# Optimization experiments

Hardware: AMD Instinct MI355X
Metric: run time of the kernel (lower is better)

Reference implementation:

```python
import math
import jax, jax.numpy as jnp
import numpy as np
from jax import lax

N_HEADS = 8
FACTOR = 5


def _pos_emb(L, d):
    pos = jnp.arange(L, dtype=jnp.float32)[:, None]
    div = jnp.exp(jnp.arange(0, d, 2, dtype=jnp.float32) * (-math.log(10000.0) / d))
    pe = jnp.zeros((L, d), jnp.float32)
    pe = pe.at[:, 0::2].set(jnp.sin(pos * div))
    pe = pe.at[:, 1::2].set(jnp.cos(pos * div))
    return pe


def _circ_conv1d(x, w, b=None):
    # x: (B, L, Cin); w: torch conv1d weight (Cout, Cin, 3); circular padding=1
    xp = jnp.concatenate([x[:, -1:], x, x[:, :1]], axis=1)
    y = lax.conv_general_dilated(xp, jnp.transpose(w, (2, 1, 0)), (1,), 'VALID',
                                 dimension_numbers=('NWC', 'WIO', 'NWC'))
    return y + b if b is not None else y


def _ln(x, g, b, eps=1e-5):
    mu = x.mean(-1, keepdims=True)
    var = ((x - mu) ** 2).mean(-1, keepdims=True)
    return (x - mu) * lax.rsqrt(var + eps) * g + b


def _prob_attn(q, k, v, key):
    # q,k,v: (b, h, L, d); self-attention so l_q == l_k == L
    b, h, L, d = q.shape
    u = min(L, int(FACTOR * math.log(L + 1)))  # sample_k == n_top
    idx = jnp.asarray(jax.random.randint(key, (L, u), 0, L))  # shared across b,h as in torch

    # sampled QK scores: scan over the u samples to avoid a (b,h,L,u,d) gather blow-up
    def step(_, idx_s):
        kg = k[:, :, idx_s]  # (b,h,L,d): key idx_s[l] for query l
        return None, jnp.einsum('bhld,bhld->bhl', q, kg)
    _, qk = lax.scan(step, None, idx.T)  # (u, b, h, L)
    qk = jnp.moveaxis(qk, 0, -1)  # (b, h, L, u)

    m = qk.max(axis=-1) - qk.mean(axis=-1)  # sparsity measure, (b,h,L)
    _, top = lax.top_k(m, u)  # (b,h,u) top-u query indices

    q_red = jnp.take_along_axis(q, top[..., None], axis=2)  # (b,h,u,d)
    scores = jnp.einsum('bhud,bhkd->bhuk', q_red, k) * (1.0 / math.sqrt(d))
    attn = jax.nn.softmax(scores, axis=-1)
    ctx_top = jnp.einsum('bhuk,bhkd->bhud', attn, v)

    # non-selected queries get mean(V); scatter sparse-attention rows back in
    ctx = jnp.broadcast_to(v.mean(axis=2, keepdims=True), (b, h, L, d))
    bi = jnp.arange(b)[:, None, None]
    hi = jnp.arange(h)[None, :, None]
    return ctx.at[bi, hi, top].set(ctx_top)


def _attn_layer(x, wq, bq, wk, bk, wv, bv, wo, bo, key):
    b, L, dm = x.shape
    dh = dm // N_HEADS
    def split(w_, b_):
        return (x @ w_.T + b_).reshape(b, L, N_HEADS, dh).transpose(0, 2, 1, 3)
    ctx = _prob_attn(split(wq, bq), split(wk, bk), split(wv, bv), key)
    ctx = ctx.transpose(0, 2, 1, 3).reshape(b, L, dm)
    return ctx @ wo.T + bo


def _conv_layer(x, w, b, g, beta):
    # circular conv -> BatchNorm (batch stats, train-mode math) -> ELU -> maxpool k3 s2 p1
    y = _circ_conv1d(x, w, b)
    mu = y.mean(axis=(0, 1))
    var = y.var(axis=(0, 1))
    y = (y - mu) * lax.rsqrt(var + 1e-5) * g + beta
    y = jax.nn.elu(y)
    yp = jnp.pad(y, ((0, 0), (1, 1), (0, 0)), constant_values=-np.inf)
    return lax.reduce_window(yp, -np.inf, lax.max, (1, 3, 1), (1, 2, 1), 'VALID')


def _forward(x, skip_w, skip_b, token_conv_w, wq, bq, wk, bk, wv, bv, wo, bo,
             w1, b1, w2, b2, ln1_g, ln1_b, ln2_g, ln2_b,
             dc_w, dc_b, bn_g, bn_b, final_ln_g, final_ln_b, proj_w, proj_b):
    skip = x[:, -1] @ skip_w.T + skip_b  # (B, pred_len)
    h = _circ_conv1d(x, token_conv_w)  # token embedding (no bias)
    h = h + _pos_emb(h.shape[1], h.shape[2])
    E = wq.shape[0]
    base = jax.random.key(42)
    for i in range(E):
        new_h = _attn_layer(h, wq[i], bq[i], wk[i], bk[i], wv[i], bv[i], wo[i], bo[i],
                            jax.random.fold_in(base, i))
        h = h + new_h
        y = _ln(h, ln1_g[i], ln1_b[i])
        y = jax.nn.gelu(y @ w1[i].T + b1[i], approximate=False)  # conv1 is 1x1
        y = y @ w2[i].T + b2[i]  # conv2 is 1x1
        h = _ln(h + y, ln2_g[i], ln2_b[i])
        if i < E - 1:
            h = _conv_layer(h, dc_w[i], dc_b[i], bn_g[i], bn_b[i])  # halves L
    h = _ln(h, final_ln_g, final_ln_b)
    return h[:, -1] @ proj_w.T + proj_b + skip


def setup_inputs() -> dict:
    B, L, C_IN, D, DFF, E, P = 32, 2048, 7, 512, 2048, 3, 96
    key = jax.random.key(0)
    ks = iter(jax.random.split(key, 20))
    w = lambda shape: jax.random.normal(next(ks), shape, jnp.float32) * 0.02
    z = lambda shape: jnp.zeros(shape, jnp.float32)
    o = lambda shape: jnp.ones(shape, jnp.float32)
    return {
        'x': jax.random.normal(next(ks), (B, L, C_IN), jnp.float32),
        'skip_w': w((P, C_IN)), 'skip_b': z((P,)),
        'token_conv_w': w((D, C_IN, 3)),
        'wq': w((E, D, D)), 'bq': z((E, D)),
        'wk': w((E, D, D)), 'bk': z((E, D)),
        'wv': w((E, D, D)), 'bv': z((E, D)),
        'wo': w((E, D, D)), 'bo': z((E, D)),
        'w1': w((E, DFF, D)), 'b1': z((E, DFF)),
        'w2': w((E, D, DFF)), 'b2': z((E, D)),
        'ln1_g': o((E, D)), 'ln1_b': z((E, D)),
        'ln2_g': o((E, D)), 'ln2_b': z((E, D)),
        'dc_w': w((E - 1, D, D, 3)), 'dc_b': z((E - 1, D)),
        'bn_g': o((E - 1, D)), 'bn_b': z((E - 1, D)),
        'final_ln_g': o((D,)), 'final_ln_b': z((D,)),
        'proj_w': w((P, D)), 'proj_b': z((P,)),
    }


def reference(x, skip_w, skip_b, token_conv_w, wq, bq, wk, bk, wv, bv, wo, bo,
              w1, b1, w2, b2, ln1_g, ln1_b, ln2_g, ln2_b,
              dc_w, dc_b, bn_g, bn_b, final_ln_g, final_ln_b, proj_w, proj_b):
    return _forward(x, skip_w, skip_b, token_conv_w, wq, bq, wk, bk, wv, bv, wo, bo,
                    w1, b1, w2, b2, ln1_g, ln1_b, ln2_g, ln2_b,
                    dc_w, dc_b, bn_g, bn_b, final_ln_g, final_ln_b, proj_w, proj_b)
```

## Files before the change

kernel.cpp:

```cpp
#include <hip/hip_runtime.h>
#include <cmath>

#define DM 512
#define DH 64

typedef __attribute__((ext_vector_type(8))) short short8;
typedef __attribute__((ext_vector_type(4))) float float4v;

__device__ inline float b2f(unsigned short u){
  union{unsigned int i; float f;} z; z.i = ((unsigned)u)<<16; return z.f;
}
__device__ inline unsigned short f2b(float f){
  unsigned int x = __float_as_uint(f);
  return (unsigned short)((x + 0x7fffu + ((x>>16)&1u)) >> 16);
}
__device__ inline unsigned cvtpk2(float a, float b){
  unsigned r; asm("v_cvt_pk_bf16_f32 %0, %1, %2" : "=v"(r) : "v"(a), "v"(b)); return r;
}

#define GLL(gp, lp) __builtin_amdgcn_global_load_lds((const __attribute__((address_space(1))) void*)(gp), \
    (__attribute__((address_space(3))) void*)(lp), 16, 0, 0)

__host__ __device__ inline void tf2x32(unsigned k0, unsigned k1, unsigned& x0, unsigned& x1){
  const unsigned ks0=k0, ks1=k1, ks2=k0^k1^0x1BD11BDAu;
  x0 += ks0; x1 += ks1;
#define TF_ROT(r) { x0 += x1; x1 = (x1<<(r))|(x1>>(32-(r))); x1 ^= x0; }
  TF_ROT(13) TF_ROT(15) TF_ROT(26) TF_ROT(6)
  x0 += ks1; x1 += ks2 + 1u;
  TF_ROT(17) TF_ROT(29) TF_ROT(16) TF_ROT(24)
  x0 += ks2; x1 += ks0 + 2u;
  TF_ROT(13) TF_ROT(15) TF_ROT(26) TF_ROT(6)
  x0 += ks0; x1 += ks1 + 3u;
  TF_ROT(17) TF_ROT(29) TF_ROT(16) TF_ROT(24)
  x0 += ks1; x1 += ks2 + 4u;
  TF_ROT(13) TF_ROT(15) TF_ROT(26) TF_ROT(6)
  x0 += ks2; x1 += ks0 + 5u;
#undef TF_ROT
}

__global__ __launch_bounds__(256) void idx_kernel(int* __restrict__ idx, unsigned k2a, unsigned k2b,
                                                  int S2, int Lmask){
  int j = blockIdx.x*256 + threadIdx.x;
  if (j >= S2) return;
  unsigned x0 = (unsigned)j, x1 = (unsigned)(S2 + j);
  tf2x32(k2a, k2b, x0, x1);
  idx[j]      = (int)(x0 & (unsigned)Lmask);
  idx[S2 + j] = (int)(x1 & (unsigned)Lmask);
}

__global__ __launch_bounds__(256) void pe_kernel(float* __restrict__ pe, int L){
  int i = blockIdx.x*256 + threadIdx.x;
  int d = i % DM, l = i / DM;
  const float scale = -0.017988946f;
  float freq = expf((float)(d & ~1) * scale);
  float ang  = (float)l * freq;
  pe[i] = (d & 1) ? cosf(ang) : sinf(ang);
}

__global__ __launch_bounds__(256) void packtcw(const float* __restrict__ tcw, float* __restrict__ tcwT){
  int i = blockIdx.x*256 + threadIdx.x;
  if (i >= 21*DM) return;
  int j = i / DM, d = i % DM;
  tcwT[(size_t)j*DM + d] = tcw[(size_t)d*21 + (j%7)*3 + (j/7)];
}

__global__ __launch_bounds__(256) void embed2(const float* __restrict__ x, const float* __restrict__ tcwT,
                                              const float* __restrict__ pe, float* __restrict__ h, int L){
  int row = blockIdx.x; int l = row % L, b = row / L;
  __shared__ float xs[21];
  int t = threadIdx.x;
  if (t < 21){
    int c = t % 7, kk = t / 7;
    int ls = l + kk - 1; ls = (ls < 0) ? ls + L : (ls >= L ? ls - L : ls);
    xs[t] = x[((size_t)b*L + ls)*7 + c];
  }
  __syncthreads();
  for (int d = t; d < DM; d += 256){
    float acc = 0.f;
#pragma unroll
    for (int j=0;j<21;j++) acc += xs[j]*tcwT[j*DM + d];
    h[(size_t)row*DM + d] = acc + pe[(size_t)l*DM + d];
  }
}

__global__ __launch_bounds__(256) void f2b_vec(const float* __restrict__ src, unsigned short* __restrict__ dst, int n4){
  int i = blockIdx.x*256 + threadIdx.x;
  if (i >= n4) return;
  float4 v = ((const float4*)src)[i];
  uint2 o; o.x = cvtpk2(v.x, v.y); o.y = cvtpk2(v.z, v.w);
  ((uint2*)dst)[i] = o;
}

__global__ __launch_bounds__(256) void packconv(const float* __restrict__ dcw, unsigned short* __restrict__ wtapK){
  int i = blockIdx.x*256 + threadIdx.x;
  if (i >= 3*DM*DM) return;
  int n = i / (3*DM); int rem = i % (3*DM); int tap = rem / DM; int c = rem % DM;
  wtapK[(size_t)n*(3*DM) + tap*DM + c] = f2b(dcw[((size_t)n*DM + c)*3 + tap]);
}

__global__ __launch_bounds__(256) void catb_kernel(const float* __restrict__ a, const float* __restrict__ b,
    const float* __restrict__ c, float* __restrict__ o){
  int i = blockIdx.x*256 + threadIdx.x;
  if (i >= 1536) return;
  o[i] = (i < 512) ? a[i] : (i < 1024 ? b[i-512] : c[i-1024]);
}

template<int TN, int A32>
__global__ __launch_bounds__(256) void bgemm2(const void* __restrict__ Ain,
    const unsigned short* __restrict__ Wb, const float* __restrict__ bias, void* __restrict__ C,
    int N, int K, int L, int convmode, int act, int outbf, int qkv, size_t bufstride, int swz){
  constexpr int NJ = TN/32;
  constexpr int BR = TN/32;
  __shared__ unsigned short As[128*64];
  __shared__ unsigned short Bs[TN*64];
  int tid = threadIdx.x;
  int w = tid >> 6, ln = tid & 63;

  int bx = blockIdx.x, by = blockIdx.y;
  if (swz){
    int XT = gridDim.x, YT = gridDim.y;
    int lid = by*XT + bx;
    int xcd = lid & 7, s = lid >> 3;
    int ych = YT >> 3;
    int CHv = ych < swz ? ych : swz;
    int yloc = s % CHv;
    int t2 = s / CHv;
    int xx = t2 % XT;
    int chunk = t2 / XT;
    by = xcd*ych + chunk*CHv + yloc;
    bx = xx;
  }
  int row0 = by*128, col0 = bx*TN;
  int KA = convmode ? 512 : K;

  long aBase[4], dPrev[4], dNext[4]; int aCol[4];
#pragma unroll
  for (int g=0; g<4; g++){
    int ch = g*256 + tid;
    int r = ch >> 3, c = ch & 7;
    int gc = c ^ (r & 7);
    int gr = row0 + r;
    aCol[g] = gc*8;
    aBase[g] = (long)gr * KA;
    if (convmode){
      int l = gr % L;
      dPrev[g] = (l==0)   ? (long)(L-1)*KA : -(long)KA;
      dNext[g] = (l==L-1) ? -(long)(L-1)*KA : (long)KA;
    } else { dPrev[g]=0; dNext[g]=0; }
  }
  long bBase[BR];
#pragma unroll
  for (int g=0; g<BR; g++){
    int ch = g*256 + tid;
    int r = ch >> 3, c = ch & 7;
    int gc = c ^ (r & 7);
    bBase[g] = (long)(col0 + r)*K + gc*8;
  }
  int raBase[4], rbBase[NJ];
#pragma unroll
  for (int i=0;i<4;i++)  raBase[i] = ((w&1)*64 + i*16 + (ln&15))*8;
#pragma unroll
  for (int j=0;j<NJ;j++) rbBase[j] = ((w>>1)*(TN/2) + j*16 + (ln&15))*8;

  float4v acc[4][NJ] = {};
  int nIter = K/64;
  const unsigned short* A16 = (const unsigned short*)Ain;
  const float* Af = (const float*)Ain;

  for (int it=0; it<nIter; it++){
    int k0 = it*64;
    int kk = convmode ? (k0 & 511) : k0;
    int seg = convmode ? (k0 >> 9) : 1;
    if (A32){
#pragma unroll
      for (int g=0; g<4; g++){
        long d = convmode ? ((seg==0) ? dPrev[g] : (seg==2 ? dNext[g] : 0)) : 0;
        const float* src = Af + aBase[g] + d + kk + aCol[g];
        float4 v0 = *(const float4*)src;
        float4 v1 = *(const float4*)(src+4);
        uint4 pk;
        pk.x = cvtpk2(v0.x, v0.y); pk.y = cvtpk2(v0.z, v0.w);
        pk.z = cvtpk2(v1.x, v1.y); pk.w = cvtpk2(v1.z, v1.w);
        *(uint4*)((char*)As + g*4096 + tid*16) = pk;
      }
    } else {
#pragma unroll
      for (int g=0; g<4; g++){
        long d = convmode ? ((seg==0) ? dPrev[g] : (seg==2 ? dNext[g] : 0)) : 0;
        GLL(A16 + aBase[g] + d + kk + aCol[g], (char*)As + g*4096 + w*1024);
      }
    }
#pragma unroll
    for (int g=0; g<BR; g++)
      GLL(Wb + bBase[g] + k0, (char*)Bs + g*4096 + w*1024);
    __syncthreads();
    const char* ab = (const char*)As;
    const char* bb = (const char*)Bs;
#pragma unroll
    for (int s=0;s<2;s++){
      int xs = (s*4 + (ln>>4)) ^ (ln&7);
      short8 af[4], bf[NJ];
#pragma unroll
      for (int i=0;i<4;i++)  af[i] = *(const short8*)(ab + (raBase[i] + xs)*16);
#pragma unroll
      for (int j=0;j<NJ;j++) bf[j] = *(const short8*)(bb + (rbBase[j] + xs)*16);
#pragma unroll
      for (int i=0;i<4;i++)
#pragma unroll
        for (int j=0;j<NJ;j++)
          acc[i][j] = __builtin_amdgcn_mfma_f32_16x16x32_bf16(af[i], bf[j], acc[i][j], 0, 0, 0);
    }
    __syncthreads();
  }

  float* Cf = (float*)C;
  unsigned short* Cb = (unsigned short*)C;
  int colb0 = col0 + (w>>1)*(TN/2) + (ln & 15);
#pragma unroll
  for (int i=0;i<4;i++){
    int growb = row0 + (w&1)*64 + i*16 + (ln>>4)*4;
#pragma unroll
    for (int j=0;j<NJ;j++){
      int colb = colb0 + j*16;
      float vv[4];
#pragma unroll
      for (int r=0;r<4;r++){
        float v = acc[i][j][r];
        if (bias) v += bias[colb];
        if (act){
          float z = 0.7978845608f * v * (1.f + 0.044715f*v*v);
          float e = __expf(2.f*z);
          v = v * (1.f - 1.f/(e + 1.f));
        }
        vv[r] = v;
      }
      if (outbf){
        unsigned p01 = cvtpk2(vv[0], vv[1]);
        unsigned p23 = cvtpk2(vv[2], vv[3]);
        unsigned short h0 = (unsigned short)p01, h1 = (unsigned short)(p01>>16);
        unsigned short h2 = (unsigned short)p23, h3 = (unsigned short)(p23>>16);
        if (qkv){
          int bsel = colb >> 9;
          size_t base = (size_t)bsel*bufstride + (colb & 511);
          Cb[base + (size_t)(growb+0)*512] = h0;
          Cb[base + (size_t)(growb+1)*512] = h1;
          Cb[base + (size_t)(growb+2)*512] = h2;
          Cb[base + (size_t)(growb+3)*512] = h3;
        } else {
          Cb[(size_t)(growb+0)*N + colb] = h0;
          Cb[(size_t)(growb+1)*N + colb] = h1;
          Cb[(size_t)(growb+2)*N + colb] = h2;
          Cb[(size_t)(growb+3)*N + colb] = h3;
        }
      } else {
#pragma unroll
        for (int r=0;r<4;r++) Cf[(size_t)(growb+r)*N + colb] = vv[r];
      }
    }
  }
}

__global__ __launch_bounds__(256) void sample_m2(const unsigned short* __restrict__ q,
    const unsigned short* __restrict__ k, const int* __restrict__ idx, float* __restrict__ m, int L, int u){
  int w = (blockIdx.x*256 + threadIdx.x) >> 6;
  int lane = threadIdx.x & 63;
  int l = w % L; int b = w / L;
  const unsigned short* qrow = q + (size_t)w*DM + lane*8;
  uint4 qq = *(const uint4*)qrow;
  float qv[8];
  qv[0]=b2f((unsigned short)(qq.x&0xffff)); qv[1]=b2f((unsigned short)(qq.x>>16));
  qv[2]=b2f((unsigned short)(qq.y&0xffff)); qv[3]=b2f((unsigned short)(qq.y>>16));
  qv[4]=b2f((unsigned short)(qq.z&0xffff)); qv[5]=b2f((unsigned short)(qq.z>>16));
  qv[6]=b2f((unsigned short)(qq.w&0xffff)); qv[7]=b2f((unsigned short)(qq.w>>16));
  const unsigned short* kb = k + (size_t)b*L*DM + lane*8;
  const int* ip = idx + (size_t)l*u;
  float mx = -1e30f, sum = 0.f;
  for (int s=0; s<u; s++){
    int kp = ip[s];
    uint4 kk = *(const uint4*)(kb + (size_t)kp*DM);
    float p;
    p  = qv[0]*b2f((unsigned short)(kk.x&0xffff)) + qv[1]*b2f((unsigned short)(kk.x>>16));
    p += qv[2]*b2f((unsigned short)(kk.y&0xffff)) + qv[3]*b2f((unsigned short)(kk.y>>16));
    p += qv[4]*b2f((unsigned short)(kk.z&0xffff)) + qv[5]*b2f((unsigned short)(kk.z>>16));
    p += qv[6]*b2f((unsigned short)(kk.w&0xffff)) + qv[7]*b2f((unsigned short)(kk.w>>16));
    p += __shfl_xor(p, 1); p += __shfl_xor(p, 2); p += __shfl_xor(p, 4);
    mx = fmaxf(mx, p); sum += p;
  }
  if ((lane & 7) == 0){
    int hh = lane >> 3;
    m[((size_t)b*8 + hh)*L + l] = mx - sum/(float)u;
  }
}

template<int NS>
__global__ __launch_bounds__(256) void topk_kernel(const float* __restrict__ m, int* __restrict__ top, int L, int u){
  int bh = blockIdx.x;
  const float* mm = m + (size_t)bh*L;
  int t = threadIdx.x;
  float v[NS];
#pragma unroll
  for (int s=0; s<NS; s++) v[s] = mm[s*256 + t];
  __shared__ float rv[4];
  __shared__ int   ri[4];
  for (int it=0; it<u; it++){
    float bv = -1e30f; int bi = 0x7fffffff;
#pragma unroll
    for (int s=0; s<NS; s++){
      float x = v[s]; int i = s*256 + t;
      if (x > bv || (x == bv && i < bi)) { bv = x; bi = i; }
    }
#pragma unroll
    for (int off=32; off; off>>=1){
      float ov = __shfl_xor(bv, off); int oi = __shfl_xor(bi, off);
      if (ov > bv || (ov == bv && oi < bi)) { bv = ov; bi = oi; }
    }
    if ((t & 63) == 0){ rv[t>>6] = bv; ri[t>>6] = bi; }
    __syncthreads();
    bv = rv[0]; bi = ri[0];
#pragma unroll
    for (int k2=1; k2<4; k2++){
      float ov = rv[k2]; int oi = ri[k2];
      if (ov > bv || (ov == bv && oi < bi)) { bv = ov; bi = oi; }
    }
    if (t == 0) top[bh*u + it] = bi;
    if ((bi & 255) == t){
      int slot = bi >> 8;
#pragma unroll
      for (int s=0; s<NS; s++) if (s == slot) v[s] = -1e31f;
    }
    __syncthreads();
  }
}

#define CMC 32
__global__ __launch_bounds__(256) void colmean1(const float* __restrict__ src, float* __restrict__ part, int L){
  int b = blockIdx.x, ch = blockIdx.y;
  int rpb = L / CMC;
  int t = threadIdx.x;
  const float* p = src + ((size_t)b*L + (size_t)ch*rpb)*DM;
  float s0 = 0.f, s1 = 0.f;
  for (int r=0; r<rpb; r++){ s0 += p[(size_t)r*DM + t]; s1 += p[(size_t)r*DM + t + 256]; }
  float* o = part + ((size_t)b*CMC + ch)*DM;
  o[t] = s0; o[t+256] = s1;
}
__global__ __launch_bounds__(256) void colmean2(const float* __restrict__ part, float* __restrict__ dst, int L){
  int i = blockIdx.x*256 + threadIdx.x;
  int d = i % DM, b = i / DM;
  float s = 0.f;
  for (int c=0; c<CMC; c++) s += part[((size_t)b*CMC + c)*DM + d];
  dst[i] = s / (float)L;
}

__global__ __launch_bounds__(256) void tiny_gemm(const float* __restrict__ A, const float* __restrict__ W,
    const float* __restrict__ bias, float* __restrict__ C, int N, int K){
  int row = blockIdx.x;
  const float* ar = A + (size_t)row*K;
  __shared__ float as[DM];
  for (int k=threadIdx.x; k<K; k+=256) as[k] = ar[k];
  __syncthreads();
  for (int n = threadIdx.x; n < N; n += 256){
    float acc = bias ? bias[n] : 0.f;
    const float* wr = W + (size_t)n*K;
    for (int k=0; k<K; k++) acc += as[k]*wr[k];
    C[(size_t)row*N + n] = acc;
  }
}

__global__ __launch_bounds__(256) void qred_kernel(const unsigned short* __restrict__ q, const int* __restrict__ top,
    float* __restrict__ qred, int L, int u, int n){
  int i = blockIdx.x*256 + threadIdx.x;
  if (i >= n) return;
  int d = i & 63; int rest = i >> 6; int j = rest % u; int bh = rest / u;
  int hh = bh & 7; int b = bh >> 3;
  int pos = top[bh*u + j];
  qred[i] = b2f(q[((size_t)b*L + pos)*DM + hh*DH + d]);
}

#define FKT 128
__global__ __launch_bounds__(256) void flash_attn(const float* __restrict__ qred,
    const unsigned short* __restrict__ kbuf, const unsigned short* __restrict__ vbuf,
    float* __restrict__ partM, float* __restrict__ partL, float* __restrict__ partA,
    int L, int u, int KS){
  int ks = blockIdx.x, bh = blockIdx.y; int b = bh >> 3, h = bh & 7;
  int t = threadIdx.x;
  __shared__ float Qs[38*64];
  __shared__ unsigned short Ks[FKT*64];
  __shared__ unsigned short Vs[FKT*64];
  __shared__ float Ss[38*FKT];
  for (int i=t;i<u*64;i+=256) Qs[i] = qred[(size_t)bh*u*64 + i];
  int lane = t & 63, w = t >> 6;
  float rm[10], rl[10], racc[10];
#pragma unroll
  for (int j=0;j<10;j++){ rm[j]=-1e30f; rl[j]=0.f; racc[j]=0.f; }
  int nk = L / KS;
  int kbase = ks*nk;
  int key = t & 127, rh = t >> 7;
  for (int kt = 0; kt < nk; kt += FKT){
    __syncthreads();
    for (int e = t; e < FKT*8; e += 256){
      int k = e >> 3, c = e & 7;
      size_t gidx = ((size_t)(b*L + kbase + kt + k))*DM + h*DH + c*8;
      *(uint4*)((char*)Ks + (size_t)(k*8 + (c ^ (k&7)))*16) = *(const uint4*)(kbuf + gidx);
      *(uint4*)((char*)Vs + (size_t)e*16) = *(const uint4*)(vbuf + gidx);
    }
    __syncthreads();
    for (int r = rh; r < u; r += 2){
      const float4* q4 = (const float4*)(Qs + r*64);
      float acc = 0.f;
#pragma unroll
// ... 163 lines not shown
  int ch = blockIdx.x*256 + threadIdx.x;
  if (ch >= DM) return;
  float s = 0.f, q = 0.f;
  for (int mb=0; mb<NB; mb++){
    s += partS[(size_t)mb*DM + ch];
    q += partQ[(size_t)mb*DM + ch];
  }
  float mu = s / (float)M;
  stats[ch] = mu;
  stats[DM + ch] = q / (float)M - mu*mu;
}

__global__ __launch_bounds__(256) void bnpool(const unsigned short* __restrict__ C, const float* __restrict__ stats,
    const float* __restrict__ g, const float* __restrict__ bta, float* __restrict__ Out,
    int L, int Lo){
  size_t i = (size_t)blockIdx.x*256 + threadIdx.x;
  int ch = (int)(i % DM);
  size_t r = i / DM;
  int lo = (int)(r % Lo);
  int b  = (int)(r / Lo);
  float mu = stats[ch];
  float rstd = rsqrtf(stats[DM+ch] + 1e-5f);
  float gg = g[ch], bb = bta[ch];
  float best = -1e30f;
#pragma unroll
  for (int t=-1; t<=1; t++){
    int li = 2*lo + t;
    if (li >= 0 && li < L){
      float v = (b2f(C[((size_t)b*L + li)*DM + ch]) - mu)*rstd*gg + bb;
      v = v > 0.f ? v : expm1f(v);
      best = fmaxf(best, v);
    }
  }
  Out[((size_t)b*Lo + lo)*DM + ch] = best;
}

__global__ __launch_bounds__(128) void final_kernel(const float* __restrict__ h, const float* __restrict__ x,
    const float* __restrict__ fg, const float* __restrict__ fb, const float* __restrict__ pw,
    const float* __restrict__ pb, const float* __restrict__ sw, const float* __restrict__ sb,
    float* __restrict__ out, int Lf, int L0){
  int b = blockIdx.x;
  const float* row = h + ((size_t)b*Lf + (Lf-1))*DM;
  __shared__ float xn[DM];
  __shared__ float rs[2], rq[2];
  int t = threadIdx.x;
  float v[4]; float s = 0.f, q = 0.f;
#pragma unroll
  for (int i=0;i<4;i++){ v[i] = row[t + i*128]; s += v[i]; q += v[i]*v[i]; }
#pragma unroll
  for (int off=32; off; off>>=1){ s += __shfl_xor(s,off); q += __shfl_xor(q,off); }
  if ((t & 63) == 0){ rs[t>>6] = s; rq[t>>6] = q; }
  __syncthreads();
  s = rs[0]+rs[1]; q = rq[0]+rq[1];
  float mu = s*(1.0f/DM), var = q*(1.0f/DM) - mu*mu;
  float r = rsqrtf(var + 1e-5f);
#pragma unroll
  for (int i=0;i<4;i++){ int d = t + i*128; xn[d] = (v[i]-mu)*r*fg[d] + fb[d]; }
  __syncthreads();
  if (t < 96){
    float acc = pb[t] + sb[t];
    const float* xr = x + ((size_t)b*L0 + (L0-1))*7;
#pragma unroll
    for (int c=0;c<7;c++) acc += xr[c]*sw[t*7+c];
    for (int d=0; d<DM; d++) acc += xn[d]*pw[(size_t)t*DM + d];
    out[b*96 + t] = acc;
  }
}

extern "C" void kernel_launch(void* const* d_in, const int* in_sizes, int n_in,
                              void* d_out, int out_size, void* d_ws, size_t ws_size,
                              hipStream_t stream){
  const float* x    = (const float*)d_in[0];
  const float* skw  = (const float*)d_in[1];
  const float* skb  = (const float*)d_in[2];
  const float* tcw  = (const float*)d_in[3];
  const float* wq   = (const float*)d_in[4];
  const float* bq   = (const float*)d_in[5];
  const float* wk   = (const float*)d_in[6];
  const float* bk   = (const float*)d_in[7];
  const float* wv   = (const float*)d_in[8];
  const float* bv   = (const float*)d_in[9];
  const float* wo   = (const float*)d_in[10];
  const float* bo   = (const float*)d_in[11];
  const float* w1   = (const float*)d_in[12];
  const float* b1   = (const float*)d_in[13];
  const float* w2   = (const float*)d_in[14];
  const float* b2   = (const float*)d_in[15];
  const float* ln1g = (const float*)d_in[16];
  const float* ln1b = (const float*)d_in[17];
  const float* ln2g = (const float*)d_in[18];
  const float* ln2b = (const float*)d_in[19];
  const float* dcw  = (const float*)d_in[20];
  const float* dcb  = (const float*)d_in[21];
  const float* bng  = (const float*)d_in[22];
  const float* bnb  = (const float*)d_in[23];
  const float* flg  = (const float*)d_in[24];
  const float* flb  = (const float*)d_in[25];
  const float* pw   = (const float*)d_in[26];
  const float* pb   = (const float*)d_in[27];

  const int B = 32, L0 = 2048, DFF = 2048;
  const int RG = 16384;
  const int RF = 8192;
  char* ws = (char*)d_ws;
  const size_t SZH  = (size_t)B*L0*DM*sizeof(float);
  const size_t SLOT = (size_t)RG*DM*sizeof(unsigned short);

  const size_t WBSZ = (size_t)(3*DM*DM + 2*DFF*DM + 3*DM*DM)*2;
  size_t small_bytes = (size_t)L0*40*4
                     + (size_t)RG*8*4
                     + (size_t)B*8*40*4
                     + (size_t)32*8*40*64*4
                     + (size_t)32*8*40*64*4
                     + 3*(size_t)B*DM*4
                     + 2*(size_t)128*DM*4
                     + (size_t)2*DM*4
                     + (size_t)1536*4
                     + (size_t)B*CMC*DM*4
                     + (size_t)L0*DM*4
                     + (size_t)21*DM*4;
  if (ws_size < SZH + 4*SLOT + WBSZ + small_bytes) return;

  float*          h   = (float*)(ws);
  unsigned short* P0  = (unsigned short*)(ws + SZH);
  unsigned short* P1  = (unsigned short*)(ws + SZH + SLOT);
  unsigned short* P2  = (unsigned short*)(ws + SZH + 2*SLOT);
  unsigned short* P3  = (unsigned short*)(ws + SZH + 3*SLOT);
  unsigned short* wb  = (unsigned short*)(ws + SZH + 4*SLOT);
  unsigned short* wqb = wb;
  unsigned short* w1b = wqb + (size_t)3*DM*DM;
  unsigned short* w2b = w1b + (size_t)DFF*DM;
  unsigned short* wtapK= w2b + (size_t)DM*DFF;
  char* sm = ws + SZH + 4*SLOT + WBSZ;
  int*   idx_buf  = (int*)sm;
  float* m_buf    = (float*)(sm + (size_t)L0*40*4);
  int*   top_all  = (int*)((char*)m_buf + (size_t)RG*8*4);
  float* qred_loc = (float*)((char*)top_all + (size_t)B*8*40*4);
  float* ctxt_all = qred_loc + (size_t)32*8*40*64;
  float* hm       = ctxt_all + (size_t)32*8*40*64;
  float* vmean    = hm + (size_t)B*DM;
  float* cw       = vmean + (size_t)B*DM;
  float* partS    = cw + (size_t)B*DM;
  float* partQ    = partS + (size_t)128*DM;
  float* stats    = partQ + (size_t)128*DM;
  float* bqkv     = stats + (size_t)2*DM;
  float* partC    = bqkv + (size_t)1536;
  float* pe_buf   = partC + (size_t)B*CMC*DM;
  float* tcwT     = pe_buf + (size_t)L0*DM;

  float* fpM = (float*)P0;
  float* fpL = fpM + (size_t)256*40;
  float* fpA = fpL + (size_t)256*40;

  auto conv_b = [&](const float* src, unsigned short* dst, size_t n){
    f2b_vec<<<(int)((n/4 + 255)/256), 256, 0, stream>>>(src, dst, (int)(n/4));
  };

  pe_kernel<<<(int)(((size_t)L0*DM)/256), 256, 0, stream>>>(pe_buf, L0);
  packtcw<<<(21*DM + 255)/256, 256, 0, stream>>>(tcw, tcwT);
  embed2<<<B*L0, 256, 0, stream>>>(x, tcwT, pe_buf, h, L0);

  int L = L0;
  for (int layer = 0; layer < 3; layer++){
    int M = B * L;
    int u = (int)(5.0 * log((double)L + 1.0));
    int G = RG / L;
    int nG = M / RG;
    int KS = L / 512;
    const float* wv_i = wv + (size_t)layer*DM*DM;  const float* bv_i = bv + (size_t)layer*DM;
    const float* wo_i = wo + (size_t)layer*DM*DM;  const float* bo_i = bo + (size_t)layer*DM;
    const float* b1_i = b1 + (size_t)layer*DFF;
    const float* b2_i = b2 + (size_t)layer*DM;

    conv_b(wq + (size_t)layer*DM*DM, wqb,                    (size_t)DM*DM);
    conv_b(wk + (size_t)layer*DM*DM, wqb + (size_t)DM*DM,    (size_t)DM*DM);
    conv_b(wv_i,                     wqb + (size_t)2*DM*DM,  (size_t)DM*DM);
    conv_b(w1 + (size_t)layer*DFF*DM, w1b, (size_t)DFF*DM);
    conv_b(w2 + (size_t)layer*DM*DFF, w2b, (size_t)DM*DFF);
    catb_kernel<<<6, 256, 0, stream>>>(bq + (size_t)layer*DM, bk + (size_t)layer*DM, bv_i, bqkv);
    if (layer < 2)
      packconv<<<(3*DM*DM + 255)/256, 256, 0, stream>>>(dcw + (size_t)layer*DM*DM*3, wtapK);

    unsigned ka = 0u, kb2 = (unsigned)layer;
    tf2x32(0u, 42u, ka, kb2);
    unsigned a0 = 0u, a1 = 2u;  tf2x32(ka, kb2, a0, a1);
    unsigned c0 = 1u, c1 = 3u;  tf2x32(ka, kb2, c0, c1);
    int S2 = L * u / 2;
    idx_kernel<<<(S2 + 255)/256, 256, 0, stream>>>(idx_buf, a1, c1, S2, L-1);

    for (int g = 0; g < nG; g++){
      const float* hg = h + (size_t)g*RG*DM;
      conv_b(hg, P0, (size_t)RG*DM);
      bgemm2<128,0><<<dim3(12, RG/128), 256, 0, stream>>>(P0, wqb, bqkv, P1,
          1536, 512, L, 0, 0, 1, 1, (size_t)RG*DM, 16);
      sample_m2<<<RG/4, 256, 0, stream>>>(P1, P2, idx_buf, m_buf, L, u);
      int* top_g = top_all + (size_t)g*G*8*u;
      if (L == 2048)      topk_kernel<8><<<G*8, 256, 0, stream>>>(m_buf, top_g, L, u);
      else if (L == 1024) topk_kernel<4><<<G*8, 256, 0, stream>>>(m_buf, top_g, L, u);
      else                topk_kernel<2><<<G*8, 256, 0, stream>>>(m_buf, top_g, L, u);
      int nqr = G*8*u*DH;
      qred_kernel<<<(nqr + 255)/256, 256, 0, stream>>>(P1, top_g, qred_loc, L, u, nqr);

      flash_attn<<<dim3(KS, G*8), 256, 0, stream>>>(qred_loc, P2, P3, fpM, fpL, fpA, L, u, KS);
      int nmg = G*8*u*64;
      flash_merge<<<(nmg + 255)/256, 256, 0, stream>>>(fpM, fpL, fpA,
          ctxt_all + (size_t)g*G*8*u*64, u, KS, nmg);
    }

    colmean1<<<dim3(B, CMC), 256, 0, stream>>>(h, partC, L);
    colmean2<<<B*DM/256, 256, 0, stream>>>(partC, hm, L);
    tiny_gemm<<<B, 256, 0, stream>>>(hm, wv_i, bv_i, vmean, DM, DM);
    tiny_gemm<<<B, 256, 0, stream>>>(vmean, wo_i, bo_i, cw, DM, DM);

    scatter_delta<<<B*8*u, 256, 0, stream>>>(ctxt_all, vmean, wo_i, top_all, h, L, u);

    unsigned short* ybuf = P0;
    unsigned short* mid  = P1;
    unsigned short* y2b  = P0 + (size_t)RF*DM;
    const float* l1g = ln1g + (size_t)layer*DM; const float* l1b = ln1b + (size_t)layer*DM;
    const float* l2g = ln2g + (size_t)layer*DM; const float* l2b = ln2b + (size_t)layer*DM;
    for (int r0 = 0; r0 < M; r0 += RF){
      ln_kernel<<<RF/4, 256, 0, stream>>>(h + (size_t)r0*DM, nullptr, 0, l1g, l1b, ybuf, 1, cw, L, r0);
      bgemm2<128,0><<<dim3(16, RF/128), 256, 0, stream>>>(ybuf, w1b, b1_i, mid,
          2048, 512, L, 0, 1, 1, 0, 0, 8);
      bgemm2<64,0><<<dim3(8, RF/128), 256, 0, stream>>>(mid, w2b, b2_i, y2b,
          512, 2048, L, 0, 0, 1, 0, 0, 4);
      ln_kernel<<<RF/4, 256, 0, stream>>>(h + (size_t)r0*DM, y2b, 1, l2g, l2b, h + (size_t)r0*DM, 0, cw, L, r0);
    }

    if (layer < 2){
      const float* db = dcb + (size_t)layer*DM;
      unsigned short* convb = P0;
      bgemm2<128,1><<<dim3(4, M/128), 256, 0, stream>>>(h, wtapK, db, convb,
          512, 1536, L, 1, 0, 1, 0, 0, 8);
      bnstat1<<<dim3(8, 128), 256, 0, stream>>>(convb, partS, partQ, M/128);
      bnstat2<<<2, 256, 0, stream>>>(partS, partQ, stats, 128, M);
      int Lo = L/2;
      bnpool<<<(int)(((size_t)B*Lo*DM)/256), 256, 0, stream>>>(convb, stats,
          bng + (size_t)layer*DM, bnb + (size_t)layer*DM, h, L, Lo);
      L = Lo;
    }
  }

  final_kernel<<<B, 128, 0, stream>>>(h, x, flg, flb, pw, pb, skw, skb, (float*)d_out, L, L0);
}
```

Measured before the change: 4.997 ms.

## Double-buffer GEMM LDS tiles and fuse fp32-to-bf16 conversion into QKV GEMM

The bf16 GEMM kernel now keeps two LDS buffers for the A and B tiles. It prefetches the next K-tile with global loads (or direct-to-LDS loads) while MFMA runs on the current tile, which leaves one barrier per iteration instead of two. The QKV projection reads the fp32 activations directly through the A32 path rather than running a separate conversion kernel first. Several XCD swizzle chunk sizes are also retuned. LDS use per block doubles, which can lower occupancy, and the A32 prefetch keeps the next tile in registers across the MFMA loop.

Result: no change. 5.000 ms (+0.0%).

```diff
diff --git a/kernel.cpp b/kernel.cpp
--- a/kernel.cpp
+++ b/kernel.cpp
@@ -111,8 +111,8 @@
     int N, int K, int L, int convmode, int act, int outbf, int qkv, size_t bufstride, int swz){
   constexpr int NJ = TN/32;
   constexpr int BR = TN/32;
-  __shared__ unsigned short As[128*64];
-  __shared__ unsigned short Bs[TN*64];
+  __shared__ unsigned short As[2][128*64];
+  __shared__ unsigned short Bs[2][TN*64];
   int tid = threadIdx.x;
   int w = tid >> 6, ln = tid & 63;
 
@@ -167,35 +167,60 @@
   const unsigned short* A16 = (const unsigned short*)Ain;
   const float* Af = (const float*)Ain;
 
+  float4 pv0[4], pv1[4];
+
+  auto loadA32 = [&](int it){
+    int k0 = it*64; int kk = convmode ? (k0 & 511) : k0; int seg = convmode ? (k0 >> 9) : 1;
+#pragma unroll
+    for (int g=0; g<4; g++){
+      long d = convmode ? ((seg==0) ? dPrev[g] : (seg==2 ? dNext[g] : 0)) : 0;
+      const float* src = Af + aBase[g] + d + kk + aCol[g];
+      pv0[g] = *(const float4*)src;
+      pv1[g] = *(const float4*)(src+4);
+    }
+  };
+  auto storeA32 = [&](int p){
+#pragma unroll
+    for (int g=0; g<4; g++){
+      uint4 pk;
+      pk.x = cvtpk2(pv0[g].x, pv0[g].y); pk.y = cvtpk2(pv0[g].z, pv0[g].w);
+      pk.z = cvtpk2(pv1[g].x, pv1[g].y); pk.w = cvtpk2(pv1[g].z, pv1[g].w);
+      *(uint4*)((char*)As[p] + g*4096 + tid*16) = pk;
+    }
+  };
+  auto issueA16 = [&](int it, int p){
+    int k0 = it*64; int kk = convmode ? (k0 & 511) : k0; int seg = convmode ? (k0 >> 9) : 1;
+#pragma unroll
+    for (int g=0; g<4; g++){
+      long d = convmode ? ((seg==0) ? dPrev[g] : (seg==2 ? dNext[g] : 0)) : 0;
+      GLL(A16 + aBase[g] + d + kk + aCol[g], (char*)As[p] + g*4096 + w*1024);
+    }
+  };
+  auto issueB = [&](int it, int p){
+    int k0 = it*64;
+#pragma unroll
+    for (int g=0; g<BR; g++)
+      GLL(Wb + bBase[g] + k0, (char*)Bs[p] + g*4096 + w*1024);
+  };
+
+  if (A32){ loadA32(0); storeA32(0); }
+  else    issueA16(0, 0);
+  issueB(0, 0);
+  asm volatile("s_waitcnt vmcnt(0) lgkmcnt(0)" ::: "memory");
+  __builtin_amdgcn_s_barrier();
+  asm volatile("" ::: "memory");
+
+  int cur = 0;
   for (int it=0; it<nIter; it++){
-    int k0 = it*64;
-    int kk = convmode ? (k0 & 511) : k0;
-    int seg = convmode ? (k0 >> 9) : 1;
-    if (A32){
-#pragma unroll
-      for (int g=0; g<4; g++){
-        long d = convmode ? ((seg==0) ? dPrev[g] : (seg==2 ? dNext[g] : 0)) : 0;
-        const float* src = Af + aBase[g] + d + kk + aCol[g];
-        float4 v0 = *(const float4*)src;
-        float4 v1 = *(const float4*)(src+4);
-        uint4 pk;
-        pk.x = cvtpk2(v0.x, v0.y); pk.y = cvtpk2(v0.z, v0.w);
-        pk.z = cvtpk2(v1.x, v1.y); pk.w = cvtpk2(v1.z, v1.w);
-        *(uint4*)((char*)As + g*4096 + tid*16) = pk;
-      }
-    } else {
-#pragma unroll
-      for (int g=0; g<4; g++){
-        long d = convmode ? ((seg==0) ? dPrev[g] : (seg==2 ? dNext[g] : 0)) : 0;
-        GLL(A16 + aBase[g] + d + kk + aCol[g], (char*)As + g*4096 + w*1024);
-      }
-    }
-#pragma unroll
-    for (int g=0; g<BR; g++)
-      GLL(Wb + bBase[g] + k0, (char*)Bs + g*4096 + w*1024);
-    __syncthreads();
-    const char* ab = (const char*)As;
-    const char* bb = (const char*)Bs;
+    int nxt = cur ^ 1;
+    bool more = (it+1 < nIter);
+    if (more){
+      if (A32) loadA32(it+1);
+      else     issueA16(it+1, nxt);
+      issueB(it+1, nxt);
+    }
+    const char* ab = (const char*)As[cur];
+    const char* bb = (const char*)Bs[cur];
 #pragma unroll
     for (int s=0;s<2;s++){
       int xs = (s*4 + (ln>>4)) ^ (ln&7);
@@ -210,7 +235,16 @@
         for (int j=0;j<NJ;j++)
           acc[i][j] = __builtin_amdgcn_mfma_f32_16x16x32_bf16(af[i], bf[j], acc[i][j], 0, 0, 0);
     }
-    __syncthreads();
+    if (more){
+      asm volatile("s_waitcnt vmcnt(0)" ::: "memory");
+      if (A32){
+        storeA32(nxt);
+        asm volatile("s_waitcnt lgkmcnt(0)" ::: "memory");
+      }
+      __builtin_amdgcn_s_barrier();
+      asm volatile("" ::: "memory");
+      cur = nxt;
+    }
   }
 
   float* Cf = (float*)C;
@@ -762,9 +796,8 @@
 
     for (int g = 0; g < nG; g++){
       const float* hg = h + (size_t)g*RG*DM;
-      conv_b(hg, P0, (size_t)RG*DM);
-      bgemm2<128,0><<<dim3(12, RG/128), 256, 0, stream>>>(P0, wqb, bqkv, P1,
-          1536, 512, L, 0, 0, 1, 1, (size_t)RG*DM, 16);
+      bgemm2<128,1><<<dim3(12, RG/128), 256, 0, stream>>>(hg, wqb, bqkv, P1,
+          1536, 512, L, 0, 0, 1, 1, (size_t)RG*DM, 4);
       sample_m2<<<RG/4, 256, 0, stream>>>(P1, P2, idx_buf, m_buf, L, u);
       int* top_g = top_all + (size_t)g*G*8*u;
       if (L == 2048)      topk_kernel<8><<<G*8, 256, 0, stream>>>(m_buf, top_g, L, u);
@@ -796,7 +829,7 @@
       bgemm2<128,0><<<dim3(16, RF/128), 256, 0, stream>>>(ybuf, w1b, b1_i, mid,
           2048, 512, L, 0, 1, 1, 0, 0, 8);
       bgemm2<64,0><<<dim3(8, RF/128), 256, 0, stream>>>(mid, w2b, b2_i, y2b,
-          512, 2048, L, 0, 0, 1, 0, 0, 4);
+          512, 2048, L, 0, 0, 1, 0, 0, 2);
       ln_kernel<<<RF/4, 256, 0, stream>>>(h + (size_t)r0*DM, y2b, 1, l2g, l2b, h + (size_t)r0*DM, 0, cw, L, r0);
     }
 
@@ -804,7 +837,7 @@
       const float* db = dcb + (size_t)layer*DM;
       unsigned short* convb = P0;
       bgemm2<128,1><<<dim3(4, M/128), 256, 0, stream>>>(h, wtapK, db, convb,
-          512, 1536, L, 1, 0, 1, 0, 0, 8);
+          512, 1536, L, 1, 0, 1, 0, 0, 4);
       bnstat1<<<dim3(8, 128), 256, 0, stream>>>(convb, partS, partQ, M/128);
       bnstat2<<<2, 256, 0, stream>>>(partS, partQ, stats, 128, M);
       int Lo = L/2;
```

## Add A-resident GEMM kernel for QKV and FFN1, fuse fp32-to-bf16 input conversion

Applied to the files above, without the earlier changes.

Adds a GEMM kernel that loads a full 128x512 A tile into LDS once and loops over several 128-column output panels, streaming only the weight tiles. It is used for the QKV projection, where it also converts the fp32 activations to bf16 while loading, which removes the separate conversion kernel. It is also used for the first FFN GEMM. The swizzle arguments of the remaining bgemm2 calls are also changed. The cost is far fewer blocks (2 or 4 in x) and 144KB of LDS per block, so occupancy drops and the grid may underfill the GPU.

Result: slower. 5.764 ms (+15.3%).

```diff
diff --git a/kernel.cpp b/kernel.cpp
--- a/kernel.cpp
+++ b/kernel.cpp
@@ -3,6 +3,8 @@
 
 #define DM 512
 #define DH 64
+#define AK 512
+#define AKC 64
 
 typedef __attribute__((ext_vector_type(8))) short short8;
 typedef __attribute__((ext_vector_type(4))) float float4v;
@@ -103,6 +105,130 @@
   int i = blockIdx.x*256 + threadIdx.x;
   if (i >= 1536) return;
   o[i] = (i < 512) ? a[i] : (i < 1024 ? b[i-512] : c[i-1024]);
+}
+
+template<int A32>
+__global__ __launch_bounds__(256) void bgemm_ares(const void* __restrict__ Ain,
+    const unsigned short* __restrict__ Wb, const float* __restrict__ bias, void* __restrict__ C,
+    int N, int NP, int act, int outbf, int qkv, size_t bufstride){
+  extern __shared__ char lds_ares[];
+  unsigned short* Ab = (unsigned short*)lds_ares;
+  char* Bsb = lds_ares + (size_t)128*AK*2;
+  int tid = threadIdx.x; int w = tid >> 6, ln = tid & 63;
+  int by = blockIdx.y, bx = blockIdx.x;
+  int row0 = by*128;
+  int col00 = bx*NP*128;
+
+  if (A32){
+    const float* Af = (const float*)Ain;
+    for (int e = tid; e < 128*AKC; e += 256){
+      int r = e >> 6, ck = e & 63;
+      const float* src = Af + (size_t)(row0 + r)*AK + ck*8;
+      float4 v0 = *(const float4*)src;
+      float4 v1 = *(const float4*)(src+4);
+      uint4 pk;
+      pk.x = cvtpk2(v0.x,v0.y); pk.y = cvtpk2(v0.z,v0.w);
+      pk.z = cvtpk2(v1.x,v1.y); pk.w = cvtpk2(v1.z,v1.w);
+      *(uint4*)((char*)Ab + ((size_t)r*AKC + (ck ^ (r&7)))*16) = pk;
+    }
+  } else {
+    const unsigned short* A16 = (const unsigned short*)Ain;
+    for (int r = w; r < 128; r += 4){
+      const unsigned short* src = A16 + (size_t)(row0 + r)*AK + (size_t)((ln ^ (r&7))*8);
+      GLL(src, (char*)Ab + (size_t)r*1024);
+    }
+  }
+  __syncthreads();
+
+  int raRow[4];
+#pragma unroll
+  for (int i=0;i<4;i++) raRow[i] = (w&1)*64 + i*16 + (ln&15);
+  int rbBase[4];
+#pragma unroll
+  for (int j=0;j<4;j++) rbBase[j] = ((w>>1)*64 + j*16 + (ln&15))*8;
+  int sR[4], sGC[4];
+#pragma unroll
+  for (int g=0; g<4; g++){
+    int ch = g*256 + tid;
+    int r = ch >> 3, c = ch & 7;
+    sR[g] = r; sGC[g] = (c ^ (r&7))*8;
+  }
+
+  float* Cf = (float*)C;
+  unsigned short* Cb = (unsigned short*)C;
+
+  for (int p = 0; p < NP; p++){
+    int col0 = col00 + p*128;
+    float4v acc[4][4] = {};
+#pragma unroll 1
+    for (int it = 0; it < 8; it++){
+      int k0 = it*64;
+#pragma unroll
+      for (int g=0; g<4; g++)
+        GLL(Wb + (size_t)(col0 + sR[g])*AK + k0 + sGC[g], Bsb + g*4096 + w*1024);
+      __syncthreads();
+#pragma unroll
+      for (int s=0;s<2;s++){
+        int sub = (s*4 + (ln>>4)) ^ (ln&7);
+        short8 af[4], bf[4];
+#pragma unroll
+        for (int i=0;i<4;i++)
+          af[i] = *(const short8*)((char*)Ab + ((size_t)raRow[i]*AKC + it*8 + sub)*16);
+#pragma unroll
+        for (int j=0;j<4;j++)
+          bf[j] = *(const short8*)(Bsb + (size_t)(rbBase[j] + ((s*4+(ln>>4)) ^ (ln&7)))*16);
+#pragma unroll
+        for (int i=0;i<4;i++)
+#pragma unroll
+          for (int j=0;j<4;j++)
+            acc[i][j] = __builtin_amdgcn_mfma_f32_16x16x32_bf16(af[i], bf[j], acc[i][j], 0, 0, 0);
+      }
+      __syncthreads();
+    }
+    int colb0 = col0 + (w>>1)*64 + (ln & 15);
+#pragma unroll
+    for (int i=0;i<4;i++){
+      int growb = row0 + (w&1)*64 + i*16 + (ln>>4)*4;
+#pragma unroll
+      for (int j=0;j<4;j++){
+        int colb = colb0 + j*16;
+        float vv[4];
+#pragma unroll
+        for (int r=0;r<4;r++){
+          float v = acc[i][j][r];
+          if (bias) v += bias[colb];
+          if (act){
+            float z = 0.7978845608f * v * (1.f + 0.044715f*v*v);
+            float e = __expf(2.f*z);
+            v = v * (1.f - 1.f/(e + 1.f));
+          }
+          vv[r] = v;
+        }
+        if (outbf){
+          unsigned p01 = cvtpk2(vv[0], vv[1]);
+          unsigned p23 = cvtpk2(vv[2], vv[3]);
+          unsigned short h0 = (unsigned short)p01, h1 = (unsigned short)(p01>>16);
+          unsigned short h2 = (unsigned short)p23, h3 = (unsigned short)(p23>>16);
+          if (qkv){
+            int bsel = colb >> 9;
+            size_t base = (size_t)bsel*bufstride + (colb & 511);
+            Cb[base + (size_t)(growb+0)*512] = h0;
+            Cb[base + (size_t)(growb+1)*512] = h1;
+            Cb[base + (size_t)(growb+2)*512] = h2;
+            Cb[base + (size_t)(growb+3)*512] = h3;
+          } else {
+            Cb[(size_t)(growb+0)*N + colb] = h0;
+            Cb[(size_t)(growb+1)*N + colb] = h1;
+            Cb[(size_t)(growb+2)*N + colb] = h2;
+            Cb[(size_t)(growb+3)*N + colb] = h3;
+          }
+        } else {
+#pragma unroll
+          for (int r=0;r<4;r++) Cf[(size_t)(growb+r)*N + colb] = vv[r];
+        }
+      }
+    }
+  }
 }
 
 template<int TN, int A32>
@@ -724,6 +850,10 @@
   float* fpL = fpM + (size_t)256*40;
   float* fpA = fpL + (size_t)256*40;
 
+  const int ARES_LDS = 128*AK*2 + 16384;
+  hipFuncSetAttribute((const void*)bgemm_ares<1>, hipFuncAttributeMaxDynamicSharedMemorySize, ARES_LDS);
+  hipFuncSetAttribute((const void*)bgemm_ares<0>, hipFuncAttributeMaxDynamicSharedMemorySize, ARES_LDS);
+
   auto conv_b = [&](const float* src, unsigned short* dst, size_t n){
     f2b_vec<<<(int)((n/4 + 255)/256), 256, 0, stream>>>(src, dst, (int)(n/4));
   };
@@ -762,9 +892,8 @@
 
     for (int g = 0; g < nG; g++){
       const float* hg = h + (size_t)g*RG*DM;
-      conv_b(hg, P0, (size_t)RG*DM);
-      bgemm2<128,0><<<dim3(12, RG/128), 256, 0, stream>>>(P0, wqb, bqkv, P1,
-          1536, 512, L, 0, 0, 1, 1, (size_t)RG*DM, 16);
+      bgemm_ares<1><<<dim3(2, RG/128), 256, ARES_LDS, stream>>>(hg, wqb, bqkv, P1,
+          1536, 6, 0, 1, 1, (size_t)RG*DM);
       sample_m2<<<RG/4, 256, 0, stream>>>(P1, P2, idx_buf, m_buf, L, u);
       int* top_g = top_all + (size_t)g*G*8*u;
       if (L == 2048)      topk_kernel<8><<<G*8, 256, 0, stream>>>(m_buf, top_g, L, u);
@@ -793,10 +922,10 @@
     const float* l2g = ln2g + (size_t)layer*DM; const float* l2b = ln2b + (size_t)layer*DM;
     for (int r0 = 0; r0 < M; r0 += RF){
       ln_kernel<<<RF/4, 256, 0, stream>>>(h + (size_t)r0*DM, nullptr, 0, l1g, l1b, ybuf, 1, cw, L, r0);
-      bgemm2<128,0><<<dim3(16, RF/128), 256, 0, stream>>>(ybuf, w1b, b1_i, mid,
-          2048, 512, L, 0, 1, 1, 0, 0, 8);
+      bgemm_ares<0><<<dim3(4, RF/128), 256, ARES_LDS, stream>>>(ybuf, w1b, b1_i, mid,
+          2048, 4, 1, 1, 0, 0);
       bgemm2<64,0><<<dim3(8, RF/128), 256, 0, stream>>>(mid, w2b, b2_i, y2b,
-          512, 2048, L, 0, 0, 1, 0, 0, 4);
+          512, 2048, L, 0, 0, 1, 0, 0, 16);
       ln_kernel<<<RF/4, 256, 0, stream>>>(h + (size_t)r0*DM, y2b, 1, l2g, l2b, h + (size_t)r0*DM, 0, cw, L, r0);
     }
 
@@ -804,7 +933,7 @@
       const float* db = dcb + (size_t)layer*DM;
       unsigned short* convb = P0;
       bgemm2<128,1><<<dim3(4, M/128), 256, 0, stream>>>(h, wtapK, db, convb,
-          512, 1536, L, 1, 0, 1, 0, 0, 8);
+          512, 1536, L, 1, 0, 1, 0, 0, 16);
       bnstat1<<<dim3(8, 128), 256, 0, stream>>>(convb, partS, partQ, M/128);
       bnstat2<<<2, 256, 0, stream>>>(partS, partQ, stats, 128, M);
       int Lo = L/2;
```

## Stage bf16 GEMM epilogue through LDS for vector stores; fuse QKV input conversion

Applied to the files above, without the earlier changes.

The bf16 output path of the GEMM now writes results into shared memory first and then emits coalesced 16-byte stores, replacing scattered 2-byte stores. The QKV GEMM reads the fp32 activations directly (A32 mode), which removes the separate fp32-to-bf16 conversion pass over the activations. The XCD swizzle chunk sizes for two GEMMs are also adjusted. The LDS reuse adds a barrier and a second pass over shared memory in the epilogue.

Measured after the change: 4.807 ms. 3.8% less time.

```diff
diff --git a/kernel.cpp b/kernel.cpp
--- a/kernel.cpp
+++ b/kernel.cpp
@@ -111,8 +111,9 @@
     int N, int K, int L, int convmode, int act, int outbf, int qkv, size_t bufstride, int swz){
   constexpr int NJ = TN/32;
   constexpr int BR = TN/32;
-  __shared__ unsigned short As[128*64];
-  __shared__ unsigned short Bs[TN*64];
+  __shared__ unsigned short LDSBUF[128*64 + TN*64];
+  unsigned short* As = LDSBUF;
+  unsigned short* Bs = LDSBUF + 128*64;
   int tid = threadIdx.x;
   int w = tid >> 6, ln = tid & 63;
 
@@ -215,46 +216,70 @@
 
   float* Cf = (float*)C;
   unsigned short* Cb = (unsigned short*)C;
-  int colb0 = col0 + (w>>1)*(TN/2) + (ln & 15);
-#pragma unroll
-  for (int i=0;i<4;i++){
-    int growb = row0 + (w&1)*64 + i*16 + (ln>>4)*4;
-#pragma unroll
-    for (int j=0;j<NJ;j++){
-      int colb = colb0 + j*16;
-      float vv[4];
-#pragma unroll
-      for (int r=0;r<4;r++){
-        float v = acc[i][j][r];
-        if (bias) v += bias[colb];
-        if (act){
-          float z = 0.7978845608f * v * (1.f + 0.044715f*v*v);
-          float e = __expf(2.f*z);
-          v = v * (1.f - 1.f/(e + 1.f));
+  if (outbf){
+    int clBase = (w>>1)*(TN/2) + (ln & 15);
+#pragma unroll
+    for (int i=0;i<4;i++){
+      int rlBase = (w&1)*64 + i*16 + (ln>>4)*4;
+#pragma unroll
+      for (int j=0;j<NJ;j++){
+        int cl = clBase + j*16;
+        int colb = col0 + cl;
+        float vv[4];
+#pragma unroll
+        for (int r=0;r<4;r++){
+          float v = acc[i][j][r];
+          if (bias) v += bias[colb];
+          if (act){
+            float z = 0.7978845608f * v * (1.f + 0.044715f*v*v);
+            float e = __expf(2.f*z);
+            v = v * (1.f - 1.f/(e + 1.f));
+          }
+          vv[r] = v;
         }
-        vv[r] = v;
-      }
-      if (outbf){
         unsigned p01 = cvtpk2(vv[0], vv[1]);
         unsigned p23 = cvtpk2(vv[2], vv[3]);
-        unsigned short h0 = (unsigned short)p01, h1 = (unsigned short)(p01>>16);
-        unsigned short h2 = (unsigned short)p23, h3 = (unsigned short)(p23>>16);
-        if (qkv){
-          int bsel = colb >> 9;
-          size_t base = (size_t)bsel*bufstride + (colb & 511);
-          Cb[base + (size_t)(growb+0)*512] = h0;
-          Cb[base + (size_t)(growb+1)*512] = h1;
-          Cb[base + (size_t)(growb+2)*512] = h2;
-          Cb[base + (size_t)(growb+3)*512] = h3;
-        } else {
-          Cb[(size_t)(growb+0)*N + colb] = h0;
-          Cb[(size_t)(growb+1)*N + colb] = h1;
-          Cb[(size_t)(growb+2)*N + colb] = h2;
-          Cb[(size_t)(growb+3)*N + colb] = h3;
+        LDSBUF[(rlBase+0)*TN + cl] = (unsigned short)p01;
+        LDSBUF[(rlBase+1)*TN + cl] = (unsigned short)(p01>>16);
+        LDSBUF[(rlBase+2)*TN + cl] = (unsigned short)p23;
+        LDSBUF[(rlBase+3)*TN + cl] = (unsigned short)(p23>>16);
+      }
+    }
+    __syncthreads();
+    constexpr int CPR = TN/8;
+#pragma unroll
+    for (int e = 0; e < 128*CPR; e += 256){
+      int idx = e + tid;
+      int rl = idx / CPR, c8 = (idx % CPR)*8;
+      uint4 val = *(const uint4*)&LDSBUF[rl*TN + c8];
+      int grow = row0 + rl;
+      int colb = col0 + c8;
+      if (qkv){
+        int bsel = colb >> 9;
+        *(uint4*)&Cb[(size_t)bsel*bufstride + (size_t)grow*512 + (colb & 511)] = val;
+      } else {
+        *(uint4*)&Cb[(size_t)grow*N + colb] = val;
+      }
+    }
+  } else {
+    int colb0 = col0 + (w>>1)*(TN/2) + (ln & 15);
+#pragma unroll
+    for (int i=0;i<4;i++){
+      int growb = row0 + (w&1)*64 + i*16 + (ln>>4)*4;
+#pragma unroll
+      for (int j=0;j<NJ;j++){
+        int colb = colb0 + j*16;
+#pragma unroll
+        for (int r=0;r<4;r++){
+          float v = acc[i][j][r];
+          if (bias) v += bias[colb];
+          if (act){
+            float z = 0.7978845608f * v * (1.f + 0.044715f*v*v);
+            float e = __expf(2.f*z);
+            v = v * (1.f - 1.f/(e + 1.f));
+          }
+          Cf[(size_t)(growb+r)*N + colb] = v;
         }
-      } else {
-#pragma unroll
-        for (int r=0;r<4;r++) Cf[(size_t)(growb+r)*N + colb] = vv[r];
       }
     }
   }
@@ -762,8 +787,7 @@
 
     for (int g = 0; g < nG; g++){
       const float* hg = h + (size_t)g*RG*DM;
-      conv_b(hg, P0, (size_t)RG*DM);
-      bgemm2<128,0><<<dim3(12, RG/128), 256, 0, stream>>>(P0, wqb, bqkv, P1,
+      bgemm2<128,1><<<dim3(12, RG/128), 256, 0, stream>>>(hg, wqb, bqkv, P1,
           1536, 512, L, 0, 0, 1, 1, (size_t)RG*DM, 16);
       sample_m2<<<RG/4, 256, 0, stream>>>(P1, P2, idx_buf, m_buf, L, u);
       int* top_g = top_all + (size_t)g*G*8*u;
@@ -796,7 +820,7 @@
       bgemm2<128,0><<<dim3(16, RF/128), 256, 0, stream>>>(ybuf, w1b, b1_i, mid,
           2048, 512, L, 0, 1, 1, 0, 0, 8);
       bgemm2<64,0><<<dim3(8, RF/128), 256, 0, stream>>>(mid, w2b, b2_i, y2b,
-          512, 2048, L, 0, 0, 1, 0, 0, 4);
+          512, 2048, L, 0, 0, 1, 0, 0, 8);
       ln_kernel<<<RF/4, 256, 0, stream>>>(h + (size_t)r0*DM, y2b, 1, l2g, l2b, h + (size_t)r0*DM, 0, cw, L, r0);
     }
 
@@ -804,7 +828,7 @@
       const float* db = dcb + (size_t)layer*DM;
       unsigned short* convb = P0;
       bgemm2<128,1><<<dim3(4, M/128), 256, 0, stream>>>(h, wtapK, db, convb,
-          512, 1536, L, 1, 0, 1, 0, 0, 8);
+          512, 1536, L, 1, 0, 1, 0, 0, 16);
       bnstat1<<<dim3(8, 128), 256, 0, stream>>>(convb, partS, partQ, M/128);
       bnstat2<<<2, 256, 0, stream>>>(partS, partQ, stats, 128, M);
       int Lo = L/2;
```
